# Optimization experiments

Measured on AMD Instinct MI355X. Metric: run time of the kernel, lower is better.

The kernel has to match this reference:

```python
import jax, jax.numpy as jnp
import numpy as np

N_HEAD = 16
SPARSE_TOPK = 64
NEG_INF = float('-inf')


def setup_inputs() -> dict:
    key = jax.random.key(0)
    ks = jax.random.split(key, 12)
    B, T, C = 4, 1024, 1024
    s = 0.02
    q = jax.random.normal(ks[0], (B, T, C), jnp.float32)
    kv = jax.random.normal(ks[1], (B, T, C), jnp.float32)  # forward asserts k == v
    tgt_mask = jnp.tril(jnp.ones((T, T), jnp.bool_)).reshape(1, 1, T, T)
    inp = {'q': q, 'k': kv, 'v': kv, 'tgt_mask': tgt_mask}
    for i, n in enumerate(['Wq', 'Wk', 'Wv', 'Wo']):
        inp[n] = jax.random.normal(ks[2 + i], (C, C), jnp.float32) * s
    for i, n in enumerate(['bq', 'bk', 'bv', 'bo']):
        inp[n] = jax.random.normal(ks[6 + i], (C,), jnp.float32) * s
    return inp


def reference(q, k, v, tgt_mask, Wq, Wk, Wv, Wo, bq, bk, bv, bo):
    B, T, C = q.shape
    H = N_HEAD
    hd = C // H
    scale = 1.0 / np.sqrt(hd).astype(np.float32)
    # QKV projections -> [B, H, T, hd]
    qh = (q @ Wq + bq).reshape(B, T, H, hd).transpose(0, 2, 1, 3)
    kh = (k @ Wk + bk).reshape(B, T, H, hd).transpose(0, 2, 1, 3)
    vh = (v @ Wv + bv).reshape(B, T, H, hd).transpose(0, 2, 1, 3)
    # full attention scores [B, H, T, T]
    att = jnp.einsum('bhtd,bhsd->bhts', qh, kh) * scale
    # causal mask: masked_fill where tgt_mask == 0
    att = jnp.where(tgt_mask[:, :, :T, :T], att, NEG_INF)
    # top-k sparse pruning: keep entries >= k-th largest per row (ties kept)
    top, _ = jax.lax.top_k(att, SPARSE_TOPK)
    vk = top[..., -1:]  # [B, H, T, 1]
    att = jnp.where(att < vk, NEG_INF, att)
    att = jax.nn.softmax(att, axis=-1)
    # dropout is identity in eval (p=0.0)
    y = jnp.einsum('bhts,bhsd->bhtd', att, vh)
    y = y.transpose(0, 2, 1, 3).reshape(B, T, C)
    return y @ Wo + bo
```

## Files before the change

kernel.cpp:

```cpp
#include <hip/hip_runtime.h>
#include <hip/hip_bf16.h>
#include <math.h>

typedef __attribute__((ext_vector_type(8))) short short8;
typedef __attribute__((ext_vector_type(4))) float f32x4;
typedef __attribute__((ext_vector_type(4))) int int4v;

#define SCL 0.1803368801111204f

static __device__ __forceinline__ unsigned short f2bf(float f) {
  unsigned u = __float_as_uint(f);
  u = u + 0x7FFFu + ((u >> 16) & 1u);
  return (unsigned short)(u >> 16);
}

static __device__ __forceinline__ float fexp2(float x) {
  float r;
  asm("v_exp_f32 %0, %1" : "=v"(r) : "v"(x));
  return r;
}

static __device__ __forceinline__ unsigned keyof(float x) {
  unsigned u = __float_as_uint(x);
  return (u & 0x80000000u) ? ~u : (u | 0x80000000u);
}
static __device__ __forceinline__ float keyinv(unsigned k) {
  unsigned u = (k & 0x80000000u) ? (k & 0x7FFFFFFFu) : ~k;
  return __uint_as_float(u);
}

#define DPP_RED_STEP(x, OP, CTRL) \
  x = OP(x, __int_as_float(__builtin_amdgcn_mov_dpp(__float_as_int(x), CTRL, 0xf, 0xf, true)))
static __device__ __forceinline__ void red_maxmin(float& mx, float& mn) {
  DPP_RED_STEP(mx, fmaxf, 0xB1); DPP_RED_STEP(mn, fminf, 0xB1);
  DPP_RED_STEP(mx, fmaxf, 0x4E); DPP_RED_STEP(mn, fminf, 0x4E);
  DPP_RED_STEP(mx, fmaxf, 0x141); DPP_RED_STEP(mn, fminf, 0x141);
  DPP_RED_STEP(mx, fmaxf, 0x140); DPP_RED_STEP(mn, fminf, 0x140);
  mx = fmaxf(mx, __shfl_xor(mx, 16)); mn = fminf(mn, __shfl_xor(mn, 16));
  mx = fmaxf(mx, __shfl_xor(mx, 32)); mn = fminf(mn, __shfl_xor(mn, 32));
}
#undef DPP_RED_STEP
static __device__ __forceinline__ float red_sum2(float s) {
#define DPP_ADD(x, CTRL) \
  x = x + __int_as_float(__builtin_amdgcn_mov_dpp(__float_as_int(x), CTRL, 0xf, 0xf, true))
  DPP_ADD(s, 0xB1); DPP_ADD(s, 0x4E); DPP_ADD(s, 0x141); DPP_ADD(s, 0x140);
#undef DPP_ADD
  s += __shfl_xor(s, 16);
  s += __shfl_xor(s, 32);
  return s;
}

static __device__ __forceinline__ int saddr(int r, int c) {
  return ((r << 12) + (c << 2)) ^ ((r & 7) << 4);
}
static __device__ __forceinline__ int paddr(int r, int c) {
  return ((r << 12) + (c << 1)) ^ ((r & 7) << 4);
}

static __device__ __forceinline__ void gld_lds16(const unsigned short* g, unsigned short* l) {
  __builtin_amdgcn_global_load_lds(
      (const __attribute__((address_space(1))) void*)g,
      (__attribute__((address_space(3))) void*)l, 16, 0, 0);
}

__global__ __launch_bounds__(256) void cvt3_k(const float* __restrict__ q,
                                              const float* __restrict__ k,
                                              const float* __restrict__ v,
                                              unsigned short* __restrict__ oq,
                                              unsigned short* __restrict__ ok,
                                              unsigned short* __restrict__ ov) {
  const int y = blockIdx.y;
  const float* in = (y == 0) ? q : (y == 1) ? k : v;
  unsigned short* out = (y == 0) ? oq : (y == 1) ? ok : ov;
  const int i = blockIdx.x * 256 + threadIdx.x;
  const f32x4* p = (const f32x4*)in + 2 * (size_t)i;
  f32x4 a = p[0], b = p[1];
  short8 r;
  r[0] = (short)f2bf(a[0]); r[1] = (short)f2bf(a[1]);
  r[2] = (short)f2bf(a[2]); r[3] = (short)f2bf(a[3]);
  r[4] = (short)f2bf(b[0]); r[5] = (short)f2bf(b[1]);
  r[6] = (short)f2bf(b[2]); r[7] = (short)f2bf(b[3]);
  ((short8*)out)[i] = r;
}

__global__ __launch_bounds__(256) void wtrans4_k(const float* __restrict__ Wq,
                                                 const float* __restrict__ Wk,
                                                 const float* __restrict__ Wv,
                                                 const float* __restrict__ Wo,
                                                 unsigned short* __restrict__ Wqt,
                                                 unsigned short* __restrict__ Wkt,
                                                 unsigned short* __restrict__ Wvt,
                                                 unsigned short* __restrict__ Wot) {
  const int z = blockIdx.z;
  const float* W = (z == 0) ? Wq : (z == 1) ? Wk : (z == 2) ? Wv : Wo;
  unsigned short* Wt = (z == 0) ? Wqt : (z == 1) ? Wkt : (z == 2) ? Wvt : Wot;
  __shared__ float tile[32][33];
  const int tx = threadIdx.x, ty = threadIdx.y;
  const int x0 = blockIdx.x * 32, y0 = blockIdx.y * 32;
#pragma unroll
  for (int j = 0; j < 4; ++j)
    tile[ty + j * 8][tx] = W[(y0 + ty + j * 8) * 1024 + x0 + tx];
  __syncthreads();
#pragma unroll
  for (int j = 0; j < 4; ++j)
    Wt[(x0 + ty + j * 8) * 1024 + (y0 + tx)] = f2bf(tile[tx][ty + j * 8]);
}

template <int MODE>
static __device__ __forceinline__ void gemm_body(unsigned short* As0, unsigned short* Bs0,
                                                 unsigned short* As1, unsigned short* Bs1,
                                                 const unsigned short* __restrict__ A,
                                                 const unsigned short* __restrict__ Bt,
                                                 const float* __restrict__ bias,
                                                 void* __restrict__ out,
                                                 const int m0, const int n0) {
  const int tid = threadIdx.x;
  const int lane = tid & 63, w = tid >> 6;
  const int wr = w >> 1, wc = w & 1;
  const int l15 = lane & 15, l4 = lane >> 4;
  f32x4 acc[4][4] = {};
  const int r0 = tid >> 2, s0 = (tid & 3) * 8;
  const int r1 = r0 + 64;
  const unsigned short* gA0 = A + (m0 + r0) * 1024 + s0;
  const unsigned short* gA1 = A + (m0 + r1) * 1024 + s0;
  const unsigned short* gB0 = Bt + (n0 + r0) * 1024 + s0;
  const unsigned short* gB1 = Bt + (n0 + r1) * 1024 + s0;
  const int oA0 = r0 * 32 + s0, oA1 = r1 * 32 + s0;

  gld_lds16(gA0, As0 + oA0);
  gld_lds16(gA1, As0 + oA1);
  gld_lds16(gB0, Bs0 + oA0);
  gld_lds16(gB1, Bs0 + oA1);
  __syncthreads();

  for (int kt = 0; kt < 32; ++kt) {
    if (kt < 31) {
      const int k0n = (kt + 1) * 32;
      unsigned short* Asn = (kt & 1) ? As0 : As1;
      unsigned short* Bsn = (kt & 1) ? Bs0 : Bs1;
      gld_lds16(gA0 + k0n, Asn + oA0);
      gld_lds16(gA1 + k0n, Asn + oA1);
      gld_lds16(gB0 + k0n, Bsn + oA0);
      gld_lds16(gB1 + k0n, Bsn + oA1);
    }
    const unsigned short* Asc = (kt & 1) ? As1 : As0;
    const unsigned short* Bsc = (kt & 1) ? Bs1 : Bs0;
    short8 af[4], bfr[4];
#pragma unroll
    for (int i = 0; i < 4; ++i) {
      af[i]  = *(const short8*)(Asc + (wr * 64 + i * 16 + l15) * 32 + l4 * 8);
      bfr[i] = *(const short8*)(Bsc + (wc * 64 + i * 16 + l15) * 32 + l4 * 8);
    }
#pragma unroll
    for (int i = 0; i < 4; ++i)
#pragma unroll
      for (int j = 0; j < 4; ++j)
        acc[i][j] = __builtin_amdgcn_mfma_f32_16x16x32_bf16(af[i], bfr[j], acc[i][j], 0, 0, 0);
    __syncthreads();
  }
#pragma unroll
  for (int i = 0; i < 4; ++i) {
#pragma unroll
    for (int j = 0; j < 4; ++j) {
      const int n = n0 + wc * 64 + j * 16 + l15;
      const float bv = bias[n];
#pragma unroll
      for (int r = 0; r < 4; ++r) {
        const int m = m0 + wr * 64 + i * 16 + l4 * 4 + r;
        const float v = acc[i][j][r] + bv;
        if (MODE == 2) {
          ((float*)out)[m * 1024 + n] = v;
        } else {
          const int bb = m >> 10, t = m & 1023, hh = n >> 6, dd = n & 63;
          const unsigned short bfv = f2bf(v);
          if (MODE == 0)
            ((unsigned short*)out)[(((bb << 4) + hh) * 1024 + t) * 64 + dd] = bfv;
          else
            ((unsigned short*)out)[(((bb << 4) + hh) * 64 + dd) * 1024 + t] = bfv;
        }
      }
    }
  }
}

__global__ __launch_bounds__(256) void gemm_qkv_k(
    const unsigned short* qbf, const unsigned short* kbf, const unsigned short* vbf,
    const unsigned short* Wqt, const unsigned short* Wkt, const unsigned short* Wvt,
    const float* bq, const float* bk, const float* bv,
    unsigned short* Qh, unsigned short* Kh, unsigned short* Vth) {
  __shared__ unsigned short As0[128 * 32], Bs0[128 * 32], As1[128 * 32], Bs1[128 * 32];
  const int bid = (int)blockIdx.x;
  const int xcd = bid & 7, idx = bid >> 3;
  const int z = idx >> 5;
  const int rem = idx & 31;
  const int m0 = (xcd * 4 + (rem >> 3)) * 128;
  const int n0 = (rem & 7) * 128;
  const unsigned short* A  = (z == 0) ? qbf : ((z == 1) ? kbf : vbf);
  const unsigned short* Bt = (z == 0) ? Wqt : ((z == 1) ? Wkt : Wvt);
  const float* bias        = (z == 0) ? bq  : ((z == 1) ? bk  : bv);
  if (z == 2) gemm_body<1>(As0, Bs0, As1, Bs1, A, Bt, bias, Vth, m0, n0);
  else        gemm_body<0>(As0, Bs0, As1, Bs1, A, Bt, bias, z ? Kh : Qh, m0, n0);
}

__global__ __launch_bounds__(256) void gemm_out_k(const unsigned short* Y,
                                                  const unsigned short* Wot,
                                                  const float* bo, float* out) {
  __shared__ unsigned short As0[128 * 32], Bs0[128 * 32], As1[128 * 32], Bs1[128 * 32];
  const int bid = (int)blockIdx.x;
  const int xcd = bid & 7, idx = bid >> 3;
  const int m0 = (xcd * 4 + (idx >> 3)) * 128;
  const int n0 = (idx & 7) * 128;
  gemm_body<2>(As0, Bs0, As1, Bs1, Y, Wot, bo, out, m0, n0);
}

__global__ __launch_bounds__(1024, 8) void attn_k(const unsigned short* __restrict__ Q,
                                                  const unsigned short* __restrict__ K,
                                                  const unsigned short* __restrict__ Vt,
                                                  unsigned short* __restrict__ Y) {
  extern __shared__ __align__(16) char smem[];
  const int tid = threadIdx.x, lane = tid & 63, w = tid >> 6;
  const int bid = (int)blockIdx.x;
  const int wk = (bid & 7) * 512 + (bid >> 3);
  const int hp = wk >> 6;
  const int tc = wk & 63;
  const int t0 = 1008 - 16 * tc;
  const int b = hp >> 4, h = hp & 15;
  const unsigned short* Qp = Q + (((b * 16 + h) * 1024) + t0) * 64;
  const unsigned short* Kh = K + (b * 16 + h) * 65536;
  const unsigned short* Vh = Vt + (b * 16 + h) * 65536;
  const int L = t0 + 16;
  const int Lpad = (L + 31) & ~31;
  const int nCT = L >> 4;
  const bool full = (L > 512);
  const int l15 = lane & 15, l4 = lane >> 4;
  float* RED3 = (float*)(smem + 65536);
  float* RED2 = (float*)(smem + 65536 + 13056);

  const short8 aq0 = *(const short8*)(Qp + l15 * 64 + l4 * 8);
  const short8 aq1 = *(const short8*)(Qp + l15 * 64 + 32 + l4 * 8);

  for (int ct = w; ct < nCT; ct += 16) {
    const int c0 = ct * 16;
    const short8 kb0 = *(const short8*)(Kh + (c0 + l15) * 64 + l4 * 8);
    const short8 kb1 = *(const short8*)(Kh + (c0 + l15) * 64 + 32 + l4 * 8);
    f32x4 acc = {0.f, 0.f, 0.f, 0.f};
    __builtin_amdgcn_s_setprio(1);
    acc = __builtin_amdgcn_mfma_f32_16x16x32_bf16(aq0, kb0, acc, 0, 0, 0);
    acc = __builtin_amdgcn_mfma_f32_16x16x32_bf16(aq1, kb1, acc, 0, 0, 0);
    __builtin_amdgcn_s_setprio(0);
    const int c = c0 + l15;
    if (ct == nCT - 1) {
#pragma unroll
      for (int r = 0; r < 4; ++r) {
        const int row = l4 * 4 + r;
        *(float*)(smem + saddr(row, c)) = (c <= t0 + row) ? acc[r] * SCL : -INFINITY;
      }
    } else {
#pragma unroll
      for (int r = 0; r < 4; ++r)
        *(float*)(smem + saddr(l4 * 4 + r, c)) = acc[r] * SCL;
    }
  }
  __syncthreads();

  const int Lr = t0 + w + 1;
  const int sbase = (w << 12) | ((lane << 3) ^ ((w & 7) << 4));
  float v[16];
#pragma unroll
  for (int p = 0; p < 8; ++p) {
    const int c = (p << 7) + (lane << 1);
    const float2 t = *(const float2*)(smem + sbase + (p << 9));
    const bool vld = c < L;
    v[2 * p]     = vld ? t.x : -INFINITY;
    v[2 * p + 1] = vld ? t.y : -INFINITY;
  }

  float lm = v[0];
#pragma unroll
  for (int i = 1; i < 16; ++i) lm = fmaxf(lm, v[i]);
  float mx = lm, mn = lm;
  red_maxmin(mx, mn);

  auto countge = [&](float tm) {
    int cnt = 0;
#pragma unroll
    for (int i = 0; i < 8; ++i) cnt += (int)__popcll(__ballot(v[i] >= tm));
    if (full) {
#pragma unroll
      for (int i = 8; i < 16; ++i) cnt += (int)__popcll(__ballot(v[i] >= tm));
    }
    return cnt;
  };

  float thr = -INFINITY;
  if (Lr > 64) {
    unsigned lo = (unsigned)__builtin_amdgcn_readfirstlane((int)keyof(mn));
    unsigned hi = (unsigned)__builtin_amdgcn_readfirstlane((int)keyof(mx)) + 1u;
    int cl = Lr, ch = 0, alt = 0;
    for (int it = 0; it < 64 && (hi - lo) > 1u; ++it) {
      const unsigned span = hi - lo;
      unsigned off;
      if (alt) off = span >> 1;
      else {
        const float fr = (float)(cl - 64) / (float)(cl - ch);
        off = (unsigned)(fr * (float)span);
        if (off < 1u) off = 1u;
        if (off > span - 1u) off = span - 1u;
      }
      alt ^= 1;
      const unsigned mid = lo + off;
      const int cnt = countge(keyinv(mid));
      if (cnt >= 64) { lo = mid; cl = cnt; if (cnt == 64) hi = mid + 1u; }
      else { hi = mid; ch = cnt; }
    }
    thr = keyinv(lo);
  }

  const int pbase = (w << 12) | ((lane << 2) ^ ((w & 7) << 4));
  float s = 0.f;
  unsigned pk[8];
#pragma unroll
  for (int p = 0; p < 4; ++p) {
    const float p0 = (v[2 * p]     >= thr) ? fexp2(v[2 * p]     - mx) : 0.f;
    const float p1 = (v[2 * p + 1] >= thr) ? fexp2(v[2 * p + 1] - mx) : 0.f;
    s += p0 + p1;
    pk[p] = (unsigned)f2bf(p0) | ((unsigned)f2bf(p1) << 16);
  }
  if (full) {
#pragma unroll
    for (int p = 4; p < 8; ++p) {
      const float p0 = (v[2 * p]     >= thr) ? fexp2(v[2 * p]     - mx) : 0.f;
      const float p1 = (v[2 * p + 1] >= thr) ? fexp2(v[2 * p + 1] - mx) : 0.f;
      s += p0 + p1;
      pk[p] = (unsigned)f2bf(p0) | ((unsigned)f2bf(p1) << 16);
    }
  }
#pragma unroll
  for (int p = 0; p < 4; ++p) {
    const int c = (p << 7) + (lane << 1);
    if (c < Lpad) *(unsigned*)(smem + pbase + (p << 8)) = pk[p];
  }
  if (full) {
#pragma unroll
    for (int p = 4; p < 8; ++p) {
      const int c = ((p & 3) << 7) + (lane << 1) + 512;
      if (c < Lpad) *(unsigned*)(smem + pbase + ((p & 3) << 8) + 1024) = pk[p];
    }
  }
  s = red_sum2(s);
  if (lane == 0) RED2[w] = 1.f / s;
  __syncthreads();

  const int nST = Lpad >> 5;
  const int qd = (nST + 3) >> 2;
  const int kseg = w >> 2;
  const int d0 = (w & 3) * 16;
  int klo = kseg * qd, khi = klo + qd;
  if (klo > nST) klo = nST;
  if (khi > nST) khi = nST;
  f32x4 acc = {0.f, 0.f, 0.f, 0.f};
  for (int st = klo; st < khi; ++st) {
    const int sb = st * 32 + l4 * 8;
    const short8 paf = *(const short8*)(smem + paddr(l15, sb));
    const short8 vb = *(const short8*)(Vh + (d0 + l15) * 1024 + sb);
    __builtin_amdgcn_s_setprio(1);
    acc = __builtin_amdgcn_mfma_f32_16x16x32_bf16(paf, vb, acc, 0, 0, 0);
    __builtin_amdgcn_s_setprio(0);
  }
  if (kseg > 0) {
#pragma unroll
    for (int r = 0; r < 4; ++r)
      RED3[((kseg - 1) * 16 + l4 * 4 + r) * 68 + d0 + l15] = acc[r];
  }
  __syncthreads();
  if (kseg == 0) {
    const int d = (h << 6) + d0 + l15;
#pragma unroll
    for (int r = 0; r < 4; ++r) {
      const int row = l4 * 4 + r;
      const int col = d0 + l15;
      float sv = acc[r] + RED3[row * 68 + col] + RED3[(16 + row) * 68 + col] +
                 RED3[(32 + row) * 68 + col];
      Y[((b << 10) + t0 + row) * 1024 + d] = f2bf(sv * RED2[row]);
    }
  }
}

extern "C" void kernel_launch(void* const* d_in, const int* in_sizes, int n_in,
                              void* d_out, int out_size, void* d_ws, size_t ws_size,
                              hipStream_t stream) {
  const float* q  = (const float*)d_in[0];
  const float* k  = (const float*)d_in[1];
  const float* v  = (const float*)d_in[2];
  const float* Wq = (const float*)d_in[4];
  const float* Wk = (const float*)d_in[5];
  const float* Wv = (const float*)d_in[6];
  const float* Wo = (const float*)d_in[7];
  const float* bq = (const float*)d_in[8];
  const float* bk = (const float*)d_in[9];
  const float* bv = (const float*)d_in[10];
  const float* bo = (const float*)d_in[11];

  char* ws = (char*)d_ws;
  const size_t MB = 1u << 20;
  unsigned short* qbf = (unsigned short*)(ws + 0 * MB);
  unsigned short* kbf = (unsigned short*)(ws + 8 * MB);
  unsigned short* vbf = (unsigned short*)(ws + 16 * MB);
  unsigned short* Wqt = (unsigned short*)(ws + 24 * MB);
  unsigned short* Wkt = (unsigned short*)(ws + 26 * MB);
  unsigned short* Wvt = (unsigned short*)(ws + 28 * MB);
  unsigned short* Wot = (unsigned short*)(ws + 30 * MB);
  unsigned short* Qh  = (unsigned short*)(ws + 32 * MB);
  unsigned short* Kh  = (unsigned short*)(ws + 40 * MB);
  unsigned short* Vth = (unsigned short*)(ws + 48 * MB);
  unsigned short* Y   = qbf;

  cvt3_k<<<dim3(2048, 3), 256, 0, stream>>>(q, k, v, qbf, kbf, vbf);
  wtrans4_k<<<dim3(32, 32, 4), dim3(32, 8), 0, stream>>>(Wq, Wk, Wv, Wo, Wqt, Wkt, Wvt, Wot);
  gemm_qkv_k<<<dim3(768), 256, 0, stream>>>(qbf, kbf, vbf, Wqt, Wkt, Wvt,
                                            bq, bk, bv, Qh, Kh, Vth);
  attn_k<<<dim3(4096), 1024, 78656, stream>>>(Qh, Kh, Vth, Y);
  gemm_out_k<<<dim3(256), 256, 0, stream>>>(Y, Wot, bo, (float*)d_out);
}
```

Measured before the change: 202.4 us.

## Replace dense P·V MFMA with sparse gather over top-k surviving entries

Instead of writing a dense bf16 probability row to LDS and running MFMA over the whole causal length, each wave ballot-compacts the surviving top-k entries (probability plus column index) into LDS. It then accumulates P·V with scalar FMAs, each lane owning one head dimension, reading V in row-major [T,hd] layout. V is now produced in the same row-major layout as Q and K rather than transposed. This avoids wasted work on masked zeros and the cross-wave reduction and barriers, at the cost of scalar FMAs and gathered global V loads instead of matrix instructions. There is also per-element ballot overhead.

```diff
diff --git a/kernel.cpp b/kernel.cpp
--- a/kernel.cpp
+++ b/kernel.cpp
@@ -52,9 +52,6 @@
 
 static __device__ __forceinline__ int saddr(int r, int c) {
   return ((r << 12) + (c << 2)) ^ ((r & 7) << 4);
-}
-static __device__ __forceinline__ int paddr(int r, int c) {
-  return ((r << 12) + (c << 1)) ^ ((r & 7) << 4);
 }
 
 static __device__ __forceinline__ void gld_lds16(const unsigned short* g, unsigned short* l) {
@@ -187,7 +184,7 @@
     const unsigned short* qbf, const unsigned short* kbf, const unsigned short* vbf,
     const unsigned short* Wqt, const unsigned short* Wkt, const unsigned short* Wvt,
     const float* bq, const float* bk, const float* bv,
-    unsigned short* Qh, unsigned short* Kh, unsigned short* Vth) {
+    unsigned short* Qh, unsigned short* Kh, unsigned short* Vtd) {
   __shared__ unsigned short As0[128 * 32], Bs0[128 * 32], As1[128 * 32], Bs1[128 * 32];
   const int bid = (int)blockIdx.x;
   const int xcd = bid & 7, idx = bid >> 3;
@@ -198,7 +195,7 @@
   const unsigned short* A  = (z == 0) ? qbf : ((z == 1) ? kbf : vbf);
   const unsigned short* Bt = (z == 0) ? Wqt : ((z == 1) ? Wkt : Wvt);
   const float* bias        = (z == 0) ? bq  : ((z == 1) ? bk  : bv);
-  if (z == 2) gemm_body<1>(As0, Bs0, As1, Bs1, A, Bt, bias, Vth, m0, n0);
+  if (z == 2) gemm_body<0>(As0, Bs0, As1, Bs1, A, Bt, bias, Vtd, m0, n0);
   else        gemm_body<0>(As0, Bs0, As1, Bs1, A, Bt, bias, z ? Kh : Qh, m0, n0);
 }
 
@@ -229,12 +226,9 @@
   const unsigned short* Kh = K + (b * 16 + h) * 65536;
   const unsigned short* Vh = Vt + (b * 16 + h) * 65536;
   const int L = t0 + 16;
-  const int Lpad = (L + 31) & ~31;
   const int nCT = L >> 4;
   const bool full = (L > 512);
   const int l15 = lane & 15, l4 = lane >> 4;
-  float* RED3 = (float*)(smem + 65536);
-  float* RED2 = (float*)(smem + 65536 + 13056);
 
   const short8 aq0 = *(const short8*)(Qp + l15 * 64 + l4 * 8);
   const short8 aq1 = *(const short8*)(Qp + l15 * 64 + 32 + l4 * 8);
@@ -316,74 +310,42 @@
     thr = keyinv(lo);
   }
 
-  const int pbase = (w << 12) | ((lane << 2) ^ ((w & 7) << 4));
+  const int lbase = w << 12;
   float s = 0.f;
-  unsigned pk[8];
-#pragma unroll
-  for (int p = 0; p < 4; ++p) {
-    const float p0 = (v[2 * p]     >= thr) ? fexp2(v[2 * p]     - mx) : 0.f;
-    const float p1 = (v[2 * p + 1] >= thr) ? fexp2(v[2 * p + 1] - mx) : 0.f;
-    s += p0 + p1;
-    pk[p] = (unsigned)f2bf(p0) | ((unsigned)f2bf(p1) << 16);
-  }
-  if (full) {
-#pragma unroll
-    for (int p = 4; p < 8; ++p) {
-      const float p0 = (v[2 * p]     >= thr) ? fexp2(v[2 * p]     - mx) : 0.f;
-      const float p1 = (v[2 * p + 1] >= thr) ? fexp2(v[2 * p + 1] - mx) : 0.f;
-      s += p0 + p1;
-      pk[p] = (unsigned)f2bf(p0) | ((unsigned)f2bf(p1) << 16);
-    }
-  }
-#pragma unroll
-  for (int p = 0; p < 4; ++p) {
-    const int c = (p << 7) + (lane << 1);
-    if (c < Lpad) *(unsigned*)(smem + pbase + (p << 8)) = pk[p];
-  }
-  if (full) {
-#pragma unroll
-    for (int p = 4; p < 8; ++p) {
-      const int c = ((p & 3) << 7) + (lane << 1) + 512;
-      if (c < Lpad) *(unsigned*)(smem + pbase + ((p & 3) << 8) + 1024) = pk[p];
-    }
+  unsigned cnt = 0;
+#pragma unroll
+  for (int i = 0; i < 16; ++i) {
+    const float p = fexp2(v[i] - mx);
+    const bool pred = (v[i] >= thr) && (v[i] > -INFINITY);
+    const unsigned long long mask = __ballot(pred);
+    const unsigned pos = cnt + (unsigned)__popcll(mask & ((1ull << lane) - 1ull));
+    if (pred) {
+      const unsigned c = (unsigned)(((i >> 1) << 7) + (lane << 1) + (i & 1));
+      *(unsigned*)(smem + lbase + (int)(pos << 2)) = ((unsigned)f2bf(p) << 16) | c;
+      s += p;
+    }
+    cnt += (unsigned)__popcll(mask);
   }
   s = red_sum2(s);
-  if (lane == 0) RED2[w] = 1.f / s;
-  __syncthreads();
-
-  const int nST = Lpad >> 5;
-  const int qd = (nST + 3) >> 2;
-  const int kseg = w >> 2;
-  const int d0 = (w & 3) * 16;
-  int klo = kseg * qd, khi = klo + qd;
-  if (klo > nST) klo = nST;
-  if (khi > nST) khi = nST;
-  f32x4 acc = {0.f, 0.f, 0.f, 0.f};
-  for (int st = klo; st < khi; ++st) {
-    const int sb = st * 32 + l4 * 8;
-    const short8 paf = *(const short8*)(smem + paddr(l15, sb));
-    const short8 vb = *(const short8*)(Vh + (d0 + l15) * 1024 + sb);
-    __builtin_amdgcn_s_setprio(1);
-    acc = __builtin_amdgcn_mfma_f32_16x16x32_bf16(paf, vb, acc, 0, 0, 0);
-    __builtin_amdgcn_s_setprio(0);
-  }
-  if (kseg > 0) {
-#pragma unroll
-    for (int r = 0; r < 4; ++r)
-      RED3[((kseg - 1) * 16 + l4 * 4 + r) * 68 + d0 + l15] = acc[r];
-  }
-  __syncthreads();
-  if (kseg == 0) {
-    const int d = (h << 6) + d0 + l15;
-#pragma unroll
-    for (int r = 0; r < 4; ++r) {
-      const int row = l4 * 4 + r;
-      const int col = d0 + l15;
-      float sv = acc[r] + RED3[row * 68 + col] + RED3[(16 + row) * 68 + col] +
-                 RED3[(32 + row) * 68 + col];
-      Y[((b << 10) + t0 + row) * 1024 + d] = f2bf(sv * RED2[row]);
-    }
-  }
+  const float inv = 1.f / s;
+
+  float acc = 0.f;
+  const unsigned short* Vrow = Vh + lane;
+  for (unsigned base = 0; base < cnt; base += 64) {
+    unsigned vslot = 0u;
+    if (base + (unsigned)lane < cnt)
+      vslot = *(const unsigned*)(smem + lbase + (int)((base + lane) << 2));
+    const unsigned m = (cnt - base < 64u) ? (cnt - base) : 64u;
+#pragma unroll 4
+    for (unsigned i = 0; i < m; ++i) {
+      const unsigned u = (unsigned)__builtin_amdgcn_readlane((int)vslot, (int)i);
+      const float p = __uint_as_float(u & 0xFFFF0000u);
+      const unsigned t = u & 1023u;
+      const float vv = __uint_as_float(((unsigned)Vrow[t << 6]) << 16);
+      acc = fmaf(p, vv, acc);
+    }
+  }
+  Y[((b << 10) + t0 + w) * 1024 + (h << 6) + lane] = f2bf(acc * inv);
 }
 
 extern "C" void kernel_launch(void* const* d_in, const int* in_sizes, int n_in,
@@ -412,13 +374,13 @@
   unsigned short* Wot = (unsigned short*)(ws + 30 * MB);
   unsigned short* Qh  = (unsigned short*)(ws + 32 * MB);
   unsigned short* Kh  = (unsigned short*)(ws + 40 * MB);
-  unsigned short* Vth = (unsigned short*)(ws + 48 * MB);
+  unsigned short* Vtd = (unsigned short*)(ws + 48 * MB);
   unsigned short* Y   = qbf;
 
   cvt3_k<<<dim3(2048, 3), 256, 0, stream>>>(q, k, v, qbf, kbf, vbf);
   wtrans4_k<<<dim3(32, 32, 4), dim3(32, 8), 0, stream>>>(Wq, Wk, Wv, Wo, Wqt, Wkt, Wvt, Wot);
   gemm_qkv_k<<<dim3(768), 256, 0, stream>>>(qbf, kbf, vbf, Wqt, Wkt, Wvt,
-                                            bq, bk, bv, Qh, Kh, Vth);
-  attn_k<<<dim3(4096), 1024, 78656, stream>>>(Qh, Kh, Vth, Y);
+                                            bq, bk, bv, Qh, Kh, Vtd);
+  attn_k<<<dim3(4096), 1024, 65536, stream>>>(Qh, Kh, Vtd, Y);
   gemm_out_k<<<dim3(256), 256, 0, stream>>>(Y, Wot, bo, (float*)d_out);
 }
```

Result: slower. 262.8 us (+29.8%).
